# Kernel optimization log

Measured on AMD Instinct MI355X. Metric: run time of the kernel, lower is better.

The kernel has to match this reference:

```python
import jax, jax.numpy as jnp
import numpy as np

N_NODES = 100000
N_EDGES = 1600000


def setup_inputs() -> dict:
    key = jax.random.key(0)
    ks = jax.random.split(key, 8)
    s = 0.1  # small init scale
    return {
        "x": jax.random.normal(ks[0], (N_NODES, 58), jnp.float32),
        "edge_index": jax.random.randint(ks[1], (2, N_EDGES), 0, N_NODES, dtype=jnp.int32),
        "Wi1": s * jax.random.normal(ks[2], (2, 58, 16), jnp.float32),
        "Wr1": s * jax.random.normal(ks[3], (2, 58, 16), jnp.float32),
        "b1": s * jax.random.normal(ks[4], (2, 16), jnp.float32),
        "Wi2": s * jax.random.normal(ks[5], (2, 16, 1), jnp.float32),
        "Wr2": s * jax.random.normal(ks[6], (2, 16, 1), jnp.float32),
        "b2": s * jax.random.normal(ks[7], (2, 1), jnp.float32),
    }


def _gcn_norm(edge_index, n_nodes):
    # PyG gcn_norm with add_self_loops=False: deg from target col, sym norm
    row, col = edge_index[0], edge_index[1]
    deg = jax.ops.segment_sum(jnp.ones((edge_index.shape[1],), jnp.float32), col,
                              num_segments=n_nodes)
    dis = jnp.where(deg > 0, jax.lax.rsqrt(jnp.maximum(deg, 1.0)), 0.0)
    return row, col, dis[row] * dis[col]  # per-edge norm


def _arma_layer(x, row, col, norm, Wi, Wr, b, n_nodes):
    # T=1, shared_weights, eval-mode (internal dropout off):
    # out_k = relu(A_hat @ (x @ Wi_k) + x @ Wr_k + b_k); mean over K stacks
    h = jnp.einsum('nf,kfo->kno', x, Wi)          # [K, N, F_out]
    msg = h[:, row, :] * norm[None, :, None]      # [K, E, F_out]
    agg = jax.vmap(lambda m: jax.ops.segment_sum(m, col, num_segments=n_nodes))(msg)
    root = jnp.einsum('nf,kfo->kno', x, Wr)       # [K, N, F_out]
    return jax.nn.relu(agg + root + b[:, None, :]).mean(axis=0)


def reference(x, edge_index, Wi1, Wr1, b1, Wi2, Wr2, b2):
    row, col, norm = _gcn_norm(edge_index, N_NODES)
    h = _arma_layer(x, row, col, norm, Wi1, Wr1, b1, N_NODES)  # conv1 (relu inside)
    h = jax.nn.relu(h)                                         # wrapper F.relu
    # F.dropout(p=0.5) is identity in eval mode
    out = _arma_layer(h, row, col, norm, Wi2, Wr2, b2, N_NODES)  # conv2
    return out  # [N, 1]
```

## Files before the change

### kernel.cpp

```cpp
#include <hip/hip_runtime.h>

#define NN 100000
#define NE 1600000

constexpr int F_IN = 58;
constexpr int FH2  = 32;
constexpr int KS   = 2;

constexpr int NB   = 782;
constexpr int NBLK = 256;
constexpr int EPB  = NE / NBLK;
constexpr int SCANN = NB * NBLK;
constexpr int SCAN_BLOCKS = (SCANN + 1023) / 1024;
constexpr int DN_NODES = 64;
constexpr int DENSE_BLOCKS = (NN + DN_NODES - 1) / DN_NODES;
constexpr int LROW = 136;

using short8 = __attribute__((ext_vector_type(8))) short;
using f32x4  = __attribute__((ext_vector_type(4))) float;

__device__ inline void splitbf(float v, short& hi, short& lo) {
    unsigned ub = __float_as_uint(v);
    unsigned short h = (unsigned short)(ub >> 16);
    float hif = __uint_as_float(((unsigned)h) << 16);
    float lof = v - hif;
    unsigned short l = (unsigned short)(__float_as_uint(lof) >> 16);
    hi = (short)h; lo = (short)l;
}

__global__ void k_prep_w(const float* __restrict__ Wi, const float* __restrict__ Wr,
                         short* __restrict__ wpre) {
    int t = threadIdx.x;
    for (int idx = t; idx < 64 * 64; idx += 256) {
        int c = idx >> 6, i = idx & 63;
        int ko = c & 31, kst = ko >> 4, o = ko & 15;
        const float* W = (c < 32) ? Wi : Wr;
        float v = (i < F_IN) ? W[(kst * F_IN + i) * 16 + o] : 0.f;
        short hi, lo; splitbf(v, hi, lo);
        wpre[c * 128 + i] = hi;
        wpre[c * 128 + 64 + i] = lo;
    }
}

__global__ void k_hist_dense1(const int* __restrict__ col, int* __restrict__ bh,
                              const float* __restrict__ x,
                              const short* __restrict__ wpre,
                              const float* __restrict__ b,
                              float* __restrict__ h1, float* __restrict__ r1) {
    __shared__ int hist[NB];
    __shared__ short sA[64 * LROW];
    __shared__ short sB[64 * LROW];
    int tid = threadIdx.x;

    if (blockIdx.x < NBLK) {
        int blk = blockIdx.x;
        for (int i = tid; i < NB; i += 256) hist[i] = 0;
        __syncthreads();
        const int2* c2p = (const int2*)&col[blk * EPB];
        for (int c = tid; c < EPB / 2; c += 256) {
            int2 cc = c2p[c];
            atomicAdd(&hist[cc.x >> 7], 1);
            atomicAdd(&hist[cc.y >> 7], 1);
        }
        __syncthreads();
        for (int i = tid; i < NB; i += 256)
            bh[i * NBLK + blk] = hist[i];
        return;
    }

    int nodeBase = (blockIdx.x - NBLK) * DN_NODES;
    for (int t = tid; t < 1024; t += 256) {
        int c = t >> 4, q8 = t & 15;
        *(short8*)&sB[c * LROW + q8 * 8] = *(const short8*)&wpre[c * 128 + q8 * 8];
    }
    for (int t = tid; t < 1024; t += 256) {
        int r = t >> 4, q4 = t & 15;
        int n = nodeBase + r;
        float v0 = 0.f, v1 = 0.f, v2 = 0.f, v3 = 0.f;
        int i0 = q4 * 4;
        if (n < NN && i0 < F_IN) {
            float2 a = *(const float2*)&x[(size_t)n * F_IN + i0];
            v0 = a.x; v1 = a.y;
            if (i0 + 2 < F_IN) {
                float2 c2 = *(const float2*)&x[(size_t)n * F_IN + i0 + 2];
                v2 = c2.x; v3 = c2.y;
            }
        }
        short h0, l0, h1s, l1s, h2s, l2s, h3s, l3s;
        splitbf(v0, h0, l0); splitbf(v1, h1s, l1s);
        splitbf(v2, h2s, l2s); splitbf(v3, h3s, l3s);
        *(short4*)&sA[r * LROW + q4 * 4]      = make_short4(h0, h1s, h2s, h3s);
        *(short4*)&sA[r * LROW + 64 + q4 * 4] = make_short4(l0, l1s, l2s, l3s);
    }
    __syncthreads();

    int lane = tid & 63, w = tid >> 6;
    int r15 = lane & 15, h4 = lane >> 4;
    const short* aB = &sA[(w * 16 + r15) * LROW];
    f32x4 acc0 = {0,0,0,0}, acc1 = {0,0,0,0}, acc2 = {0,0,0,0}, acc3 = {0,0,0,0};
    const int kaA[6] = {0, 32, 0, 32, 64, 96};
    const int kaB[6] = {0, 32, 64, 96, 0, 32};
#pragma unroll
    for (int s = 0; s < 6; s++) {
        short8 af = *(const short8*)&aB[kaA[s] + h4 * 8];
#define BMM(nt, accv) { \
        short8 bf = *(const short8*)&sB[(nt * 16 + r15) * LROW + kaB[s] + h4 * 8]; \
        accv = __builtin_amdgcn_mfma_f32_16x16x32_bf16(af, bf, accv, 0, 0, 0); }
        BMM(0, acc0) BMM(1, acc1) BMM(2, acc2) BMM(3, acc3)
#undef BMM
    }
    int nb0 = nodeBase + w * 16 + h4 * 4;
#define WH(nt, accv) { int colg = nt * 16 + r15; \
    if (nb0 + 0 < NN) h1[(size_t)(nb0 + 0) * 32 + colg] = accv[0]; \
    if (nb0 + 1 < NN) h1[(size_t)(nb0 + 1) * 32 + colg] = accv[1]; \
    if (nb0 + 2 < NN) h1[(size_t)(nb0 + 2) * 32 + colg] = accv[2]; \
    if (nb0 + 3 < NN) h1[(size_t)(nb0 + 3) * 32 + colg] = accv[3]; }
#define WR(nt, accv) { int colg = nt * 16 + r15 - 32; float bv = b[colg]; \
    if (nb0 + 0 < NN) r1[(size_t)(nb0 + 0) * 32 + colg] = accv[0] + bv; \
    if (nb0 + 1 < NN) r1[(size_t)(nb0 + 1) * 32 + colg] = accv[1] + bv; \
    if (nb0 + 2 < NN) r1[(size_t)(nb0 + 2) * 32 + colg] = accv[2] + bv; \
    if (nb0 + 3 < NN) r1[(size_t)(nb0 + 3) * 32 + colg] = accv[3] + bv; }
    WH(0, acc0) WH(1, acc1) WR(2, acc2) WR(3, acc3)
#undef WH
#undef WR
}

__global__ void k_scan1(int* __restrict__ bh, int* __restrict__ bsum) {
    __shared__ int ts[256];
    int tid = threadIdx.x;
    int base = blockIdx.x * 1024 + tid * 4;
    int v0 = (base + 0 < SCANN) ? bh[base + 0] : 0;
    int v1 = (base + 1 < SCANN) ? bh[base + 1] : 0;
    int v2 = (base + 2 < SCANN) ? bh[base + 2] : 0;
    int v3 = (base + 3 < SCANN) ? bh[base + 3] : 0;
    int p0 = v0, p1 = p0 + v1, p2 = p1 + v2, p3 = p2 + v3;
    ts[tid] = p3;
    __syncthreads();
    for (int off = 1; off < 256; off <<= 1) {
        int v = (tid >= off) ? ts[tid - off] : 0;
        __syncthreads();
        ts[tid] += v;
        __syncthreads();
    }
    int prev = (tid > 0) ? ts[tid - 1] : 0;
    if (base + 0 < SCANN) bh[base + 0] = prev + p0;
    if (base + 1 < SCANN) bh[base + 1] = prev + p1;
    if (base + 2 < SCANN) bh[base + 2] = prev + p2;
    if (base + 3 < SCANN) bh[base + 3] = prev + p3;
    if (tid == 255) bsum[blockIdx.x] = ts[255];
}

__global__ void k_scan2(const int* __restrict__ bsum, int* __restrict__ boff) {
    __shared__ int s[256];
    int tid = threadIdx.x;
    s[tid] = (tid < SCAN_BLOCKS) ? bsum[tid] : 0;
    __syncthreads();
    for (int off = 1; off < 256; off <<= 1) {
        int v = (tid >= off) ? s[tid - off] : 0;
        __syncthreads();
        s[tid] += v;
        __syncthreads();
    }
    if (tid < SCAN_BLOCKS) boff[tid] = (tid > 0) ? s[tid - 1] : 0;
}

__global__ void k_bscatter(const int* __restrict__ row, const int* __restrict__ col,
                           const int* __restrict__ bh, const int* __restrict__ boff,
                           int* __restrict__ ebuck) {
    __shared__ int cur[NB];
    int tid = threadIdx.x, blk = blockIdx.x;
    for (int i = tid; i < NB; i += 256) {
        int idx = i * NBLK + blk;
        cur[i] = (idx == 0) ? 0 : bh[idx - 1] + boff[(idx - 1) >> 10];
    }
    __syncthreads();
    int base = blk * EPB;
    const int2* c2p = (const int2*)&col[base];
    const int2* r2p = (const int2*)&row[base];
    for (int c = tid; c < EPB / 2; c += 256) {
        int2 cc = c2p[c];
        int2 rr = r2p[c];
        int p0 = atomicAdd(&cur[cc.x >> 7], 1);
        ebuck[p0] = (rr.x << 7) | (cc.x & 127);
        int p1 = atomicAdd(&cur[cc.y >> 7], 1);
        ebuck[p1] = (rr.y << 7) | (cc.y & 127);
    }
}

__global__ void __launch_bounds__(256) k_bcsr_a(const int* __restrict__ bh,
                                                const int* __restrict__ boff,
                                                const int* __restrict__ ebuck,
                                                int* __restrict__ inc, float* __restrict__ dis) {
    __shared__ int cnt[258];
    __shared__ int scn[128];
    int b = blockIdx.x, tid = threadIdx.x;
    int i0 = b * NBLK - 1, i1 = (b + 1) * NBLK - 1;
    int start = (b == 0) ? 0 : bh[i0] + boff[i0 >> 10];
    int end   = bh[i1] + boff[i1 >> 10];
    if (tid < 129) { cnt[tid] = 0; cnt[129 + tid] = 0; }
    __syncthreads();
    int c0 = (tid & 1) * 129;
    for (int j = start + tid; j < end; j += 256)
        atomicAdd(&cnt[c0 + (ebuck[j] & 127)], 1);
    __syncthreads();
    int v = 0;
    if (tid < 128) { v = cnt[tid] + cnt[129 + tid]; scn[tid] = v; }
    __syncthreads();
    for (int off = 1; off < 128; off <<= 1) {
        int t = (tid < 128 && tid >= off) ? scn[tid - off] : 0;
        __syncthreads();
        if (tid < 128) scn[tid] += t;
        __syncthreads();
    }
    if (tid < 128) {
        int colIdx = (b << 7) + tid;
        if (colIdx < NN) {
            inc[colIdx] = start + scn[tid];
            dis[colIdx] = (v > 0) ? rsqrtf((float)v) : 0.f;
        }
    }
}

__global__ void __launch_bounds__(256) k_bcsr_b(const int* __restrict__ bh,
                                                const int* __restrict__ boff,
                                                const int* __restrict__ ebuck,
                                                const int* __restrict__ inc,
                                                const float* __restrict__ dis,
                                                int2* __restrict__ esrc8) {
    __shared__ int cur[128];
    __shared__ float sdis[128];
    int b = blockIdx.x, tid = threadIdx.x;
    int i0 = b * NBLK - 1, i1 = (b + 1) * NBLK - 1;
    int start = (b == 0) ? 0 : bh[i0] + boff[i0 >> 10];
    int end   = bh[i1] + boff[i1 >> 10];
    if (tid < 128) {
        int colIdx = (b << 7) + tid;
        cur[tid]  = (colIdx == 0) ? 0 : ((colIdx <= NN) ? inc[colIdx - 1] : 0);
        sdis[tid] = (colIdx < NN) ? dis[colIdx] : 0.f;
    }
    __syncthreads();
    for (int j = start + tid; j < end; j += 256) {
        int e = ebuck[j];
        int c = e & 127, s = e >> 7;
        int pos = atomicAdd(&cur[c], 1);
        float w = dis[s] * sdis[c];
        esrc8[pos] = make_int2(s, __float_as_int(w));
    }
}

__global__ void k_gather1_mid(const int* __restrict__ inc, const int2* __restrict__ esrc8,
                              const float4* __restrict__ h1, const float4* __restrict__ r1,
                              const float4* __restrict__ Wi2, const float4* __restrict__ Wr2,
                              const float* __restrict__ b2,
                              float* __restrict__ h2, float* __restrict__ r2) {
    int tid = blockIdx.x * blockDim.x + threadIdx.x;
    int n = tid >> 3, l = tid & 7;
    if (n >= NN) return;
    int js = (n == 0) ? 0 : inc[n - 1];
    int je = inc[n];
    float4 acc = r1[(size_t)n * 8 + l];
    int j = js;
#define EDGE1(ss, ww) { \
        float4 v = h1[(size_t)(ss) * 8 + l]; \
        acc.x = fmaf(ww, v.x, acc.x); acc.y = fmaf(ww, v.y, acc.y); \
        acc.z = fmaf(ww, v.z, acc.z); acc.w = fmaf(ww, v.w, acc.w); }
    if ((j & 1) && j < je) {
        int2 e = esrc8[j];
        EDGE1(e.x, __int_as_float(e.y))
        j++;
    }
    for (; j + 3 < je; j += 4) {
        int4 ep0 = *(const int4*)&esrc8[j];
        int4 ep1 = *(const int4*)&esrc8[j + 2];
        EDGE1(ep0.x, __int_as_float(ep0.y))
        EDGE1(ep0.z, __int_as_float(ep0.w))
        EDGE1(ep1.x, __int_as_float(ep1.y))
        EDGE1(ep1.z, __int_as_float(ep1.w))
    }
    for (; j + 1 < je; j += 2) {
        int4 ep = *(const int4*)&esrc8[j];
        EDGE1(ep.x, __int_as_float(ep.y))
        EDGE1(ep.z, __int_as_float(ep.w))
    }
    if (j < je) {
        int2 e = esrc8[j];
        EDGE1(e.x, __int_as_float(e.y))
    }
#undef EDGE1
    acc.x = fmaxf(acc.x, 0.f); acc.y = fmaxf(acc.y, 0.f);
    acc.z = fmaxf(acc.z, 0.f); acc.w = fmaxf(acc.w, 0.f);
    float4 h;
    h.x = 0.5f * (acc.x + __shfl_xor(acc.x, 4));
    h.y = 0.5f * (acc.y + __shfl_xor(acc.y, 4));
    h.z = 0.5f * (acc.z + __shfl_xor(acc.z, 4));
    h.w = 0.5f * (acc.w + __shfl_xor(acc.w, 4));
    float4 wi = Wi2[l], wr = Wr2[l];
    float p1 = h.x * wi.x + h.y * wi.y + h.z * wi.z + h.w * wi.w;
    float p2 = h.x * wr.x + h.y * wr.y + h.z * wr.z + h.w * wr.w;
    p1 += __shfl_xor(p1, 1); p1 += __shfl_xor(p1, 2);
    p2 += __shfl_xor(p2, 1); p2 += __shfl_xor(p2, 2);
    if ((l & 3) == 0) {
        int k = l >> 2;
        h2[n * 2 + k] = p1;
        r2[n * 2 + k] = p2 + b2[k];
    }
}

__global__ void k_gather2(const int* __restrict__ inc, const int2* __restrict__ esrc8,
                          const float* __restrict__ h2, const float* __restrict__ r2,
                          float* __restrict__ out) {
    int tid = blockIdx.x * blockDim.x + threadIdx.x;
    int n = tid >> 2, l = tid & 3;
    if (n >= NN) return;
    int js = (n == 0) ? 0 : inc[n - 1];
    int je = inc[n];
    float a0 = 0.f, a1v = 0.f;
    for (int j = js + l; j < je; j += 4) {
        int2 e = esrc8[j];
        float w = __int_as_float(e.y);
        float2 hv = *(const float2*)&h2[(size_t)e.x * 2];
        a0  = fmaf(w, hv.x, a0);
        a1v = fmaf(w, hv.y, a1v);
    }
    a0  += __shfl_xor(a0, 1);  a0  += __shfl_xor(a0, 2);
    a1v += __shfl_xor(a1v, 1); a1v += __shfl_xor(a1v, 2);
    if (l == 0) {
        float2 rv = *(const float2*)&r2[(size_t)n * 2];
        out[n] = 0.5f * (fmaxf(a0 + rv.x, 0.f) + fmaxf(a1v + rv.y, 0.f));
    }
}

extern "C" void kernel_launch(void* const* d_in, const int* in_sizes, int n_in,
                              void* d_out, int out_size, void* d_ws, size_t ws_size,
                              hipStream_t stream) {
    const float* x   = (const float*)d_in[0];
    const int*   ei  = (const int*)d_in[1];
    const float* Wi1 = (const float*)d_in[2];
    const float* Wr1 = (const float*)d_in[3];
    const float* b1  = (const float*)d_in[4];
    const float* Wi2 = (const float*)d_in[5];
    const float* Wr2 = (const float*)d_in[6];
    const float* b2  = (const float*)d_in[7];
    float* out = (float*)d_out;

    const int* row = ei;
    const int* col = ei + NE;

    int*   bh    = (int*)d_ws;
    int*   bsum  = bh + SCANN;
    int*   boff  = bsum + 256;
    float* dis   = (float*)(boff + 256);
    int*   inc   = (int*)(dis + NN);
    short* wpre  = (short*)(inc + NN);
    int*   ebuck = (int*)(wpre + 8192);
    int2*  esrc8 = (int2*)(ebuck + NE);
    float* h1    = (float*)(esrc8 + NE);
    float* r1    = h1 + (size_t)NN * FH2;
    float* h2    = r1 + (size_t)NN * FH2;
    float* r2    = h2 + (size_t)NN * KS;

    const int B = 256;
    k_prep_w<<<1, B, 0, stream>>>(Wi1, Wr1, wpre);
    k_hist_dense1<<<NBLK + DENSE_BLOCKS, B, 0, stream>>>(col, bh, x, wpre, b1, h1, r1);
    k_scan1<<<SCAN_BLOCKS, B, 0, stream>>>(bh, bsum);
    k_scan2<<<1, 256, 0, stream>>>(bsum, boff);
    k_bscatter<<<NBLK, B, 0, stream>>>(row, col, bh, boff, ebuck);
    k_bcsr_a<<<NB, B, 0, stream>>>(bh, boff, ebuck, inc, dis);
    k_bcsr_b<<<NB, B, 0, stream>>>(bh, boff, ebuck, inc, dis, esrc8);
    k_gather1_mid<<<(NN * 8 + B - 1) / B, B, 0, stream>>>(inc, esrc8,
        (const float4*)h1, (const float4*)r1, (const float4*)Wi2, (const float4*)Wr2,
        b2, h2, r2);
    k_gather2<<<(NN * 4 + B - 1) / B, B, 0, stream>>>(inc, esrc8, h2, r2, out);
}
```

Baseline: 112.2 us.

## Store layer-1 gather features as bf16 and raise histogram block count

The layer-1 node features h1, which are gathered once per edge, are now stored as round-to-nearest bf16 instead of fp32. This halves the bytes read in the dominant gather kernel, which now uses 4 lanes per node with 8 features each instead of 8 lanes with 4. The histogram and scatter block count goes from 256 to 500, and the scan2 kernel is widened to 512 threads to cover the larger number of scan blocks. The 4-edge unrolled loop is removed. The cost is bf16 rounding error in the aggregated messages, and each lane now carries more work, which may reduce latency hiding.

```diff
diff --git a/kernel.cpp b/kernel.cpp
--- a/kernel.cpp
+++ b/kernel.cpp
@@ -8,7 +8,7 @@
 constexpr int KS   = 2;
 
 constexpr int NB   = 782;
-constexpr int NBLK = 256;
+constexpr int NBLK = 500;
 constexpr int EPB  = NE / NBLK;
 constexpr int SCANN = NB * NBLK;
 constexpr int SCAN_BLOCKS = (SCANN + 1023) / 1024;
@@ -26,6 +26,16 @@
     float lof = v - hif;
     unsigned short l = (unsigned short)(__float_as_uint(lof) >> 16);
     hi = (short)h; lo = (short)l;
+}
+
+__device__ inline unsigned short bf16rne(float v) {
+    unsigned u = __float_as_uint(v);
+    unsigned r = u + 0x7FFF + ((u >> 16) & 1);
+    return (unsigned short)(r >> 16);
+}
+
+__device__ inline float bf2f(unsigned short s) {
+    return __uint_as_float(((unsigned)s) << 16);
 }
 
 __global__ void k_prep_w(const float* __restrict__ Wi, const float* __restrict__ Wr,
@@ -46,7 +56,7 @@
                               const float* __restrict__ x,
                               const short* __restrict__ wpre,
                               const float* __restrict__ b,
-                              float* __restrict__ h1, float* __restrict__ r1) {
+                              unsigned short* __restrict__ h1b, float* __restrict__ r1) {
     __shared__ int hist[NB];
     __shared__ short sA[64 * LROW];
     __shared__ short sB[64 * LROW];
@@ -111,10 +121,10 @@
     }
     int nb0 = nodeBase + w * 16 + h4 * 4;
 #define WH(nt, accv) { int colg = nt * 16 + r15; \
-    if (nb0 + 0 < NN) h1[(size_t)(nb0 + 0) * 32 + colg] = accv[0]; \
-    if (nb0 + 1 < NN) h1[(size_t)(nb0 + 1) * 32 + colg] = accv[1]; \
-    if (nb0 + 2 < NN) h1[(size_t)(nb0 + 2) * 32 + colg] = accv[2]; \
-    if (nb0 + 3 < NN) h1[(size_t)(nb0 + 3) * 32 + colg] = accv[3]; }
+    if (nb0 + 0 < NN) h1b[(size_t)(nb0 + 0) * 32 + colg] = bf16rne(accv[0]); \
+    if (nb0 + 1 < NN) h1b[(size_t)(nb0 + 1) * 32 + colg] = bf16rne(accv[1]); \
+    if (nb0 + 2 < NN) h1b[(size_t)(nb0 + 2) * 32 + colg] = bf16rne(accv[2]); \
+    if (nb0 + 3 < NN) h1b[(size_t)(nb0 + 3) * 32 + colg] = bf16rne(accv[3]); }
 #define WR(nt, accv) { int colg = nt * 16 + r15 - 32; float bv = b[colg]; \
     if (nb0 + 0 < NN) r1[(size_t)(nb0 + 0) * 32 + colg] = accv[0] + bv; \
     if (nb0 + 1 < NN) r1[(size_t)(nb0 + 1) * 32 + colg] = accv[1] + bv; \
@@ -151,11 +161,11 @@
 }
 
 __global__ void k_scan2(const int* __restrict__ bsum, int* __restrict__ boff) {
-    __shared__ int s[256];
+    __shared__ int s[512];
     int tid = threadIdx.x;
     s[tid] = (tid < SCAN_BLOCKS) ? bsum[tid] : 0;
     __syncthreads();
-    for (int off = 1; off < 256; off <<= 1) {
+    for (int off = 1; off < 512; off <<= 1) {
         int v = (tid >= off) ? s[tid - off] : 0;
         __syncthreads();
         s[tid] += v;
@@ -249,34 +259,34 @@
 }
 
 __global__ void k_gather1_mid(const int* __restrict__ inc, const int2* __restrict__ esrc8,
-                              const float4* __restrict__ h1, const float4* __restrict__ r1,
+                              const unsigned short* __restrict__ h1b,
+                              const float4* __restrict__ r1,
                               const float4* __restrict__ Wi2, const float4* __restrict__ Wr2,
                               const float* __restrict__ b2,
                               float* __restrict__ h2, float* __restrict__ r2) {
     int tid = blockIdx.x * blockDim.x + threadIdx.x;
-    int n = tid >> 3, l = tid & 7;
+    int n = tid >> 2, l = tid & 3;
     if (n >= NN) return;
     int js = (n == 0) ? 0 : inc[n - 1];
     int je = inc[n];
-    float4 acc = r1[(size_t)n * 8 + l];
+    float4 accA = r1[(size_t)n * 8 + l * 2];
+    float4 accB = r1[(size_t)n * 8 + l * 2 + 1];
     int j = js;
 #define EDGE1(ss, ww) { \
-        float4 v = h1[(size_t)(ss) * 8 + l]; \
-        acc.x = fmaf(ww, v.x, acc.x); acc.y = fmaf(ww, v.y, acc.y); \
-        acc.z = fmaf(ww, v.z, acc.z); acc.w = fmaf(ww, v.w, acc.w); }
+        short8 hv = *(const short8*)&h1b[(size_t)(ss) * 32 + l * 8]; \
+        accA.x = fmaf(ww, bf2f((unsigned short)hv[0]), accA.x); \
+        accA.y = fmaf(ww, bf2f((unsigned short)hv[1]), accA.y); \
+        accA.z = fmaf(ww, bf2f((unsigned short)hv[2]), accA.z); \
+        accA.w = fmaf(ww, bf2f((unsigned short)hv[3]), accA.w); \
+        accB.x = fmaf(ww, bf2f((unsigned short)hv[4]), accB.x); \
+        accB.y = fmaf(ww, bf2f((unsigned short)hv[5]), accB.y); \
+        accB.z = fmaf(ww, bf2f((unsigned short)hv[6]), accB.z); \
+        accB.w = fmaf(ww, bf2f((unsigned short)hv[7]), accB.w); }
     if ((j & 1) && j < je) {
         int2 e = esrc8[j];
         EDGE1(e.x, __int_as_float(e.y))
         j++;
     }
-    for (; j + 3 < je; j += 4) {
-        int4 ep0 = *(const int4*)&esrc8[j];
-        int4 ep1 = *(const int4*)&esrc8[j + 2];
-        EDGE1(ep0.x, __int_as_float(ep0.y))
-        EDGE1(ep0.z, __int_as_float(ep0.w))
-        EDGE1(ep1.x, __int_as_float(ep1.y))
-        EDGE1(ep1.z, __int_as_float(ep1.w))
-    }
     for (; j + 1 < je; j += 2) {
         int4 ep = *(const int4*)&esrc8[j];
         EDGE1(ep.x, __int_as_float(ep.y))
@@ -287,20 +297,29 @@
         EDGE1(e.x, __int_as_float(e.y))
     }
 #undef EDGE1
-    acc.x = fmaxf(acc.x, 0.f); acc.y = fmaxf(acc.y, 0.f);
-    acc.z = fmaxf(acc.z, 0.f); acc.w = fmaxf(acc.w, 0.f);
-    float4 h;
-    h.x = 0.5f * (acc.x + __shfl_xor(acc.x, 4));
-    h.y = 0.5f * (acc.y + __shfl_xor(acc.y, 4));
-    h.z = 0.5f * (acc.z + __shfl_xor(acc.z, 4));
-    h.w = 0.5f * (acc.w + __shfl_xor(acc.w, 4));
-    float4 wi = Wi2[l], wr = Wr2[l];
-    float p1 = h.x * wi.x + h.y * wi.y + h.z * wi.z + h.w * wi.w;
-    float p2 = h.x * wr.x + h.y * wr.y + h.z * wr.z + h.w * wr.w;
-    p1 += __shfl_xor(p1, 1); p1 += __shfl_xor(p1, 2);
-    p2 += __shfl_xor(p2, 1); p2 += __shfl_xor(p2, 2);
-    if ((l & 3) == 0) {
-        int k = l >> 2;
+    accA.x = fmaxf(accA.x, 0.f); accA.y = fmaxf(accA.y, 0.f);
+    accA.z = fmaxf(accA.z, 0.f); accA.w = fmaxf(accA.w, 0.f);
+    accB.x = fmaxf(accB.x, 0.f); accB.y = fmaxf(accB.y, 0.f);
+    accB.z = fmaxf(accB.z, 0.f); accB.w = fmaxf(accB.w, 0.f);
+    float4 hA, hB;
+    hA.x = 0.5f * (accA.x + __shfl_xor(accA.x, 2));
+    hA.y = 0.5f * (accA.y + __shfl_xor(accA.y, 2));
+    hA.z = 0.5f * (accA.z + __shfl_xor(accA.z, 2));
+    hA.w = 0.5f * (accA.w + __shfl_xor(accA.w, 2));
+    hB.x = 0.5f * (accB.x + __shfl_xor(accB.x, 2));
+    hB.y = 0.5f * (accB.y + __shfl_xor(accB.y, 2));
+    hB.z = 0.5f * (accB.z + __shfl_xor(accB.z, 2));
+    hB.w = 0.5f * (accB.w + __shfl_xor(accB.w, 2));
+    float4 wiA = Wi2[l * 2], wiB = Wi2[l * 2 + 1];
+    float4 wrA = Wr2[l * 2], wrB = Wr2[l * 2 + 1];
+    float p1 = hA.x * wiA.x + hA.y * wiA.y + hA.z * wiA.z + hA.w * wiA.w
+             + hB.x * wiB.x + hB.y * wiB.y + hB.z * wiB.z + hB.w * wiB.w;
+    float p2 = hA.x * wrA.x + hA.y * wrA.y + hA.z * wrA.z + hA.w * wrA.w
+             + hB.x * wrB.x + hB.y * wrB.y + hB.z * wrB.z + hB.w * wrB.w;
+    p1 += __shfl_xor(p1, 1);
+    p2 += __shfl_xor(p2, 1);
+    if ((l & 1) == 0) {
+        int k = l >> 1;
         h2[n * 2 + k] = p1;
         r2[n * 2 + k] = p2 + b2[k];
     }
@@ -348,27 +367,26 @@
 
     int*   bh    = (int*)d_ws;
     int*   bsum  = bh + SCANN;
-    int*   boff  = bsum + 256;
-    float* dis   = (float*)(boff + 256);
+    int*   boff  = bsum + 512;
+    float* dis   = (float*)(boff + 512);
     int*   inc   = (int*)(dis + NN);
     short* wpre  = (short*)(inc + NN);
     int*   ebuck = (int*)(wpre + 8192);
     int2*  esrc8 = (int2*)(ebuck + NE);
-    float* h1    = (float*)(esrc8 + NE);
-    float* r1    = h1 + (size_t)NN * FH2;
+    unsigned short* h1b = (unsigned short*)(esrc8 + NE);
+    float* r1    = (float*)(h1b + (size_t)NN * FH2);
     float* h2    = r1 + (size_t)NN * FH2;
     float* r2    = h2 + (size_t)NN * KS;
 
     const int B = 256;
     k_prep_w<<<1, B, 0, stream>>>(Wi1, Wr1, wpre);
-    k_hist_dense1<<<NBLK + DENSE_BLOCKS, B, 0, stream>>>(col, bh, x, wpre, b1, h1, r1);
+    k_hist_dense1<<<NBLK + DENSE_BLOCKS, B, 0, stream>>>(col, bh, x, wpre, b1, h1b, r1);
     k_scan1<<<SCAN_BLOCKS, B, 0, stream>>>(bh, bsum);
-    k_scan2<<<1, 256, 0, stream>>>(bsum, boff);
+    k_scan2<<<1, 512, 0, stream>>>(bsum, boff);
     k_bscatter<<<NBLK, B, 0, stream>>>(row, col, bh, boff, ebuck);
     k_bcsr_a<<<NB, B, 0, stream>>>(bh, boff, ebuck, inc, dis);
     k_bcsr_b<<<NB, B, 0, stream>>>(bh, boff, ebuck, inc, dis, esrc8);
-    k_gather1_mid<<<(NN * 8 + B - 1) / B, B, 0, stream>>>(inc, esrc8,
-        (const float4*)h1, (const float4*)r1, (const float4*)Wi2, (const float4*)Wr2,
-        b2, h2, r2);
+    k_gather1_mid<<<(NN * 4 + B - 1) / B, B, 0, stream>>>(inc, esrc8, h1b,
+        (const float4*)r1, (const float4*)Wi2, (const float4*)Wr2, b2, h2, r2);
     k_gather2<<<(NN * 4 + B - 1) / B, B, 0, stream>>>(inc, esrc8, h2, r2, out);
 }
```

New measurement: 126.7 us. +13.0%, slower.

## Store layer-1 messages as bf16 and raise histogram block count

Applied to the files above, without the earlier changes.

The per-node layer-1 message features h1 are now rounded to bf16 (round-to-nearest-even) when written, and the edge gather in k_gather1_mid reads them as short4 and widens them back to float. This halves the bytes of the random per-edge gather, which is the main memory cost of layer 1. The histogram and bucket-scatter partitioning goes from 256 to 500 blocks for more parallelism, and the scan2 kernel is widened to 512 threads to cover the larger scan. The cost is reduced precision in the aggregated messages, and the larger block count enlarges the prefix-scan work.

```diff
diff --git a/kernel.cpp b/kernel.cpp
--- a/kernel.cpp
+++ b/kernel.cpp
@@ -8,7 +8,7 @@
 constexpr int KS   = 2;
 
 constexpr int NB   = 782;
-constexpr int NBLK = 256;
+constexpr int NBLK = 500;
 constexpr int EPB  = NE / NBLK;
 constexpr int SCANN = NB * NBLK;
 constexpr int SCAN_BLOCKS = (SCANN + 1023) / 1024;
@@ -26,6 +26,16 @@
     float lof = v - hif;
     unsigned short l = (unsigned short)(__float_as_uint(lof) >> 16);
     hi = (short)h; lo = (short)l;
+}
+
+__device__ inline unsigned short bf16rne(float v) {
+    unsigned u = __float_as_uint(v);
+    unsigned r = u + 0x7FFF + ((u >> 16) & 1);
+    return (unsigned short)(r >> 16);
+}
+
+__device__ inline float bf2f(unsigned short s) {
+    return __uint_as_float(((unsigned)s) << 16);
 }
 
 __global__ void k_prep_w(const float* __restrict__ Wi, const float* __restrict__ Wr,
@@ -46,7 +56,7 @@
                               const float* __restrict__ x,
                               const short* __restrict__ wpre,
                               const float* __restrict__ b,
-                              float* __restrict__ h1, float* __restrict__ r1) {
+                              unsigned short* __restrict__ h1b, float* __restrict__ r1) {
     __shared__ int hist[NB];
     __shared__ short sA[64 * LROW];
     __shared__ short sB[64 * LROW];
@@ -111,10 +121,10 @@
     }
     int nb0 = nodeBase + w * 16 + h4 * 4;
 #define WH(nt, accv) { int colg = nt * 16 + r15; \
-    if (nb0 + 0 < NN) h1[(size_t)(nb0 + 0) * 32 + colg] = accv[0]; \
-    if (nb0 + 1 < NN) h1[(size_t)(nb0 + 1) * 32 + colg] = accv[1]; \
-    if (nb0 + 2 < NN) h1[(size_t)(nb0 + 2) * 32 + colg] = accv[2]; \
-    if (nb0 + 3 < NN) h1[(size_t)(nb0 + 3) * 32 + colg] = accv[3]; }
+    if (nb0 + 0 < NN) h1b[(size_t)(nb0 + 0) * 32 + colg] = bf16rne(accv[0]); \
+    if (nb0 + 1 < NN) h1b[(size_t)(nb0 + 1) * 32 + colg] = bf16rne(accv[1]); \
+    if (nb0 + 2 < NN) h1b[(size_t)(nb0 + 2) * 32 + colg] = bf16rne(accv[2]); \
+    if (nb0 + 3 < NN) h1b[(size_t)(nb0 + 3) * 32 + colg] = bf16rne(accv[3]); }
 #define WR(nt, accv) { int colg = nt * 16 + r15 - 32; float bv = b[colg]; \
     if (nb0 + 0 < NN) r1[(size_t)(nb0 + 0) * 32 + colg] = accv[0] + bv; \
     if (nb0 + 1 < NN) r1[(size_t)(nb0 + 1) * 32 + colg] = accv[1] + bv; \
@@ -151,11 +161,11 @@
 }
 
 __global__ void k_scan2(const int* __restrict__ bsum, int* __restrict__ boff) {
-    __shared__ int s[256];
+    __shared__ int s[512];
     int tid = threadIdx.x;
     s[tid] = (tid < SCAN_BLOCKS) ? bsum[tid] : 0;
     __syncthreads();
-    for (int off = 1; off < 256; off <<= 1) {
+    for (int off = 1; off < 512; off <<= 1) {
         int v = (tid >= off) ? s[tid - off] : 0;
         __syncthreads();
         s[tid] += v;
@@ -249,7 +259,8 @@
 }
 
 __global__ void k_gather1_mid(const int* __restrict__ inc, const int2* __restrict__ esrc8,
-                              const float4* __restrict__ h1, const float4* __restrict__ r1,
+                              const unsigned short* __restrict__ h1b,
+                              const float4* __restrict__ r1,
                               const float4* __restrict__ Wi2, const float4* __restrict__ Wr2,
                               const float* __restrict__ b2,
                               float* __restrict__ h2, float* __restrict__ r2) {
@@ -261,9 +272,11 @@
     float4 acc = r1[(size_t)n * 8 + l];
     int j = js;
 #define EDGE1(ss, ww) { \
-        float4 v = h1[(size_t)(ss) * 8 + l]; \
-        acc.x = fmaf(ww, v.x, acc.x); acc.y = fmaf(ww, v.y, acc.y); \
-        acc.z = fmaf(ww, v.z, acc.z); acc.w = fmaf(ww, v.w, acc.w); }
+        short4 hv = *(const short4*)&h1b[(size_t)(ss) * 32 + l * 4]; \
+        acc.x = fmaf(ww, bf2f((unsigned short)hv.x), acc.x); \
+        acc.y = fmaf(ww, bf2f((unsigned short)hv.y), acc.y); \
+        acc.z = fmaf(ww, bf2f((unsigned short)hv.z), acc.z); \
+        acc.w = fmaf(ww, bf2f((unsigned short)hv.w), acc.w); }
     if ((j & 1) && j < je) {
         int2 e = esrc8[j];
         EDGE1(e.x, __int_as_float(e.y))
@@ -348,27 +361,26 @@
 
     int*   bh    = (int*)d_ws;
     int*   bsum  = bh + SCANN;
-    int*   boff  = bsum + 256;
-    float* dis   = (float*)(boff + 256);
+    int*   boff  = bsum + 512;
+    float* dis   = (float*)(boff + 512);
     int*   inc   = (int*)(dis + NN);
     short* wpre  = (short*)(inc + NN);
     int*   ebuck = (int*)(wpre + 8192);
     int2*  esrc8 = (int2*)(ebuck + NE);
-    float* h1    = (float*)(esrc8 + NE);
-    float* r1    = h1 + (size_t)NN * FH2;
+    unsigned short* h1b = (unsigned short*)(esrc8 + NE);
+    float* r1    = (float*)(h1b + (size_t)NN * FH2);
     float* h2    = r1 + (size_t)NN * FH2;
     float* r2    = h2 + (size_t)NN * KS;
 
     const int B = 256;
     k_prep_w<<<1, B, 0, stream>>>(Wi1, Wr1, wpre);
-    k_hist_dense1<<<NBLK + DENSE_BLOCKS, B, 0, stream>>>(col, bh, x, wpre, b1, h1, r1);
+    k_hist_dense1<<<NBLK + DENSE_BLOCKS, B, 0, stream>>>(col, bh, x, wpre, b1, h1b, r1);
     k_scan1<<<SCAN_BLOCKS, B, 0, stream>>>(bh, bsum);
-    k_scan2<<<1, 256, 0, stream>>>(bsum, boff);
+    k_scan2<<<1, 512, 0, stream>>>(bsum, boff);
     k_bscatter<<<NBLK, B, 0, stream>>>(row, col, bh, boff, ebuck);
     k_bcsr_a<<<NB, B, 0, stream>>>(bh, boff, ebuck, inc, dis);
     k_bcsr_b<<<NB, B, 0, stream>>>(bh, boff, ebuck, inc, dis, esrc8);
-    k_gather1_mid<<<(NN * 8 + B - 1) / B, B, 0, stream>>>(inc, esrc8,
-        (const float4*)h1, (const float4*)r1, (const float4*)Wi2, (const float4*)Wr2,
-        b2, h2, r2);
+    k_gather1_mid<<<(NN * 8 + B - 1) / B, B, 0, stream>>>(inc, esrc8, h1b,
+        (const float4*)r1, (const float4*)Wi2, (const float4*)Wr2, b2, h2, r2);
     k_gather2<<<(NN * 4 + B - 1) / B, B, 0, stream>>>(inc, esrc8, h2, r2, out);
 }
```

Result: slower. 120.2 us (+7.1%).
